# Kernel optimization log

Hardware: AMD Instinct MI355X
Metric: run time of the kernel (lower is better)

Reference implementation:

```python
import jax, jax.numpy as jnp
import numpy as np

NUM_HEADS = 16
HEAD_DIM = 64
MODEL_DIM = NUM_HEADS * HEAD_DIM  # 1024
N_TOKENS = 121
BATCH = 1024
DISTURB_HEADS = np.array([0, 3], dtype=int)


def setup_inputs() -> dict:
    key = jax.random.key(0)
    ks = jax.random.split(key, 8)
    scale = 1.0 / np.sqrt(MODEL_DIM)
    return {
        "query": jax.random.normal(ks[0], (BATCH, MODEL_DIM), dtype=jnp.float32),
        "key": jax.random.normal(ks[1], (BATCH, N_TOKENS, MODEL_DIM), dtype=jnp.float32),
        "value": jax.random.normal(ks[2], (BATCH, N_TOKENS, MODEL_DIM), dtype=jnp.float32),
        "Wq": jax.random.normal(ks[3], (MODEL_DIM, MODEL_DIM), dtype=jnp.float32) * scale,
        "bq": jnp.zeros((MODEL_DIM,), dtype=jnp.float32),
        "Wk": jax.random.normal(ks[4], (MODEL_DIM, MODEL_DIM), dtype=jnp.float32) * scale,
        "bk": jnp.zeros((MODEL_DIM,), dtype=jnp.float32),
        "Wv": jax.random.normal(ks[5], (MODEL_DIM, MODEL_DIM), dtype=jnp.float32) * scale,
        "bv": jnp.zeros((MODEL_DIM,), dtype=jnp.float32),
    }


def reference(query, key, value, Wq, bq, Wk, bk, Wv, bv):
    B, N, _ = key.shape
    H, d = NUM_HEADS, HEAD_DIM
    # Linear projections (plain GEMMs)
    q_proj = query @ Wq + bq            # [B, H*d]
    k_proj = key @ Wk + bk              # [B, N, H*d]
    v_proj = value @ Wv + bv            # [B, N, H*d]

    q = q_proj.reshape(B, H, d)         # [B, H, d]
    k = k_proj.reshape(B, N, H, d)      # [B, N, H, d]
    v = v_proj.reshape(B, N, H, d)

    # single-query scores per head: [B, H, N]
    scores = jnp.einsum('bhd,bnhd->bhn', q, k)
    # head-wise disturb override: masked heads get all-ones scores
    mask = jnp.zeros((H,), dtype=bool).at[DISTURB_HEADS].set(True)[None, :, None]
    scores = jnp.where(mask, jnp.ones_like(scores), scores)
    # note: original scales by sqrt(d * H), not sqrt(d)
    scores = scores / jnp.sqrt(jnp.asarray(d * H, dtype=scores.dtype))
    weights = jax.nn.softmax(scores, axis=-1)   # [B, H, N]
    output = jnp.einsum('bhn,bnhd->bhd', weights, v).reshape(B, H * d)
    return (output, weights)
```

## Files before the change

kernel.cpp:

```cpp
#include <hip/hip_runtime.h>
#include <hip/hip_bf16.h>

#define NHEADS 16
#define HDIM   64
#define MDIM   1024
#define NTOK   121
#define NBATCH 1024

typedef __attribute__((ext_vector_type(4))) float f32x4;
typedef __attribute__((ext_vector_type(4))) short s16x4;
typedef __attribute__((ext_vector_type(8))) short s16x8;

#define WAIT_VM(n)  asm volatile("s_waitcnt vmcnt(" #n ")" ::: "memory")
#define WAIT_LGKM0() asm volatile("s_waitcnt lgkmcnt(0)" ::: "memory")

__device__ __forceinline__ short f2bf(float f) {
  __hip_bfloat16 h = __float2bfloat16(f);
  return __builtin_bit_cast(short, h);
}

#define GLDS(gptr, lptr)                                                        \
  __builtin_amdgcn_global_load_lds(                                             \
      (const __attribute__((address_space(1))) void*)(gptr),                    \
      (__attribute__((address_space(3))) void*)(lptr), 16, 0, 0)

__global__ __launch_bounds__(256) void kTransW(const float* __restrict__ Wq,
                                               const float* __restrict__ Wk,
                                               const float* __restrict__ Wv,
                                               short* __restrict__ Wt) {
  int bid = blockIdx.x;
  int m = bid >> 8, tile = bid & 255;
  int tr = tile >> 4, tc = tile & 15;
  const float* W = (m == 0) ? Wq : (m == 1) ? Wk : Wv;
  short* T = Wt + (size_t)m * (MDIM * MDIM);
  __shared__ float tl[64][68];
  int t = threadIdx.x;
  int c4 = t & 15, r0 = t >> 4;
#pragma unroll
  for (int i = 0; i < 4; ++i) {
    int kr = r0 + i * 16;
    f32x4 v = *(const f32x4*)(W + (size_t)(tr * 64 + kr) * MDIM + tc * 64 + c4 * 4);
    *(f32x4*)&tl[kr][c4 * 4] = v;
  }
  __syncthreads();
#pragma unroll
  for (int i = 0; i < 4; ++i) {
    int n = r0 + i * 16;
    s16x4 o;
    o.x = f2bf(tl[c4 * 4 + 0][n]);
    o.y = f2bf(tl[c4 * 4 + 1][n]);
    o.z = f2bf(tl[c4 * 4 + 2][n]);
    o.w = f2bf(tl[c4 * 4 + 3][n]);
    *(s16x4*)(T + (size_t)(tc * 64 + n) * MDIM + tr * 64 + c4 * 4) = o;
  }
}

__device__ __forceinline__ void gemm_core(const float* __restrict__ A, int mrows,
                                          const short* __restrict__ Wt, int c0,
                                          short* Alds, short* Bl0, short* Bl1,
                                          f32x4 acc[4][4], int t) {
  int wid = t >> 6, lane = t & 63;
  int wr = wid >> 1, wc = wid & 1;
  int li = lane & 15, lg = lane >> 4;
  int kq = t & 15, r0s = t >> 4;
#pragma unroll
  for (int fm = 0; fm < 4; ++fm)
#pragma unroll
    for (int fn = 0; fn < 4; ++fn) acc[fm][fn] = (f32x4)0.0f;

  int rhi[4];
#pragma unroll
  for (int i = 0; i < 4; ++i) {
    int row = r0s + 64 + (i << 4);
    rhi[i] = row < mrows ? row : mrows - 1;
  }
#pragma unroll
  for (int i = 0; i < 4; ++i) {
    int cl = wid * 32 + i * 8 + (lane >> 3);
    int jg = (lane & 7) ^ (cl & 7);
    GLDS(Wt + (size_t)(c0 + cl) * MDIM + jg * 8, Bl0 + (wid * 32 + i * 8) * 64);
  }
  f32x4 rLo[4];
#pragma unroll
  for (int i = 0; i < 4; ++i)
    rLo[i] = *(const f32x4*)(A + (size_t)(r0s + (i << 4)) * MDIM + kq * 4);

  for (int kt = 0; kt < 16; ++kt) {
    int k0 = kt * 64;
    short* Bcur = (kt & 1) ? Bl1 : Bl0;
    short* Bnxt = (kt & 1) ? Bl0 : Bl1;
    int kn = (kt < 15) ? k0 + 64 : 0;

    f32x4 rHi[4];
#pragma unroll
    for (int i = 0; i < 4; ++i)
      rHi[i] = *(const f32x4*)(A + (size_t)rhi[i] * MDIM + k0 + kq * 4);

    WAIT_VM(4);
    __builtin_amdgcn_s_barrier();
#pragma unroll
    for (int i = 0; i < 4; ++i) {
      int row = r0s + (i << 4);
      s16x4 b4;
      b4.x = f2bf(rLo[i].x); b4.y = f2bf(rLo[i].y);
      b4.z = f2bf(rLo[i].z); b4.w = f2bf(rLo[i].w);
      int byte = (row * 128 + kq * 8) ^ ((row & 7) << 4);
      *(s16x4*)((char*)Alds + byte) = b4;
    }
#pragma unroll
    for (int i = 0; i < 4; ++i) {
      int cl = wid * 32 + i * 8 + (lane >> 3);
      int jg = (lane & 7) ^ (cl & 7);
      GLDS(Wt + (size_t)(c0 + cl) * MDIM + kn + jg * 8, Bnxt + (wid * 32 + i * 8) * 64);
    }
    WAIT_VM(4);
#pragma unroll
    for (int i = 0; i < 4; ++i) {
      int row = r0s + 64 + (i << 4);
      s16x4 b4;
      b4.x = f2bf(rHi[i].x); b4.y = f2bf(rHi[i].y);
      b4.z = f2bf(rHi[i].z); b4.w = f2bf(rHi[i].w);
      int byte = (row * 128 + kq * 8) ^ ((row & 7) << 4);
      *(s16x4*)((char*)Alds + byte) = b4;
    }
#pragma unroll
    for (int i = 0; i < 4; ++i)
      rLo[i] = *(const f32x4*)(A + (size_t)(r0s + (i << 4)) * MDIM + kn + kq * 4);

    WAIT_LGKM0();
    __builtin_amdgcn_s_barrier();
#pragma unroll
    for (int ks = 0; ks < 2; ++ks) {
      s16x8 af[4];
      int kb = ks * 64 + lg * 16;
#pragma unroll
      for (int fm = 0; fm < 4; ++fm) {
        int row = wr * 64 + fm * 16 + li;
        int byte = (row * 128 + kb) ^ ((row & 7) << 4);
        af[fm] = *(s16x8*)((char*)Alds + byte);
      }
#pragma unroll
      for (int fn = 0; fn < 4; ++fn) {
        int col = wc * 64 + fn * 16 + li;
        int byte = (col * 128 + kb) ^ ((col & 7) << 4);
        s16x8 bfv = *(s16x8*)((char*)Bcur + byte);
#pragma unroll
        for (int fm = 0; fm < 4; ++fm)
          acc[fm][fn] = __builtin_amdgcn_mfma_f32_16x16x32_bf16(af[fm], bfv,
                                                                acc[fm][fn], 0, 0, 0);
      }
    }
  }
}

__global__ __launch_bounds__(256, 3) void kQProj(const float* __restrict__ query,
                                                 const short* __restrict__ WtQ,
                                                 const float* __restrict__ bq,
                                                 float* __restrict__ qp) {
  __shared__ alignas(16) short Alds[128 * 64];
  __shared__ alignas(16) short Bl0[128 * 64];
  __shared__ alignas(16) short Bl1[128 * 64];
  int bid = blockIdx.x;
  int rt = bid >> 3, ct = bid & 7;
  f32x4 acc[4][4];
  int t = threadIdx.x;
  gemm_core(query + (size_t)rt * 128 * MDIM, 128, WtQ, ct * 128, Alds, Bl0, Bl1, acc, t);
  int wid = t >> 6, lane = t & 63;
  int wr = wid >> 1, wc = wid & 1, li = lane & 15, lg = lane >> 4;
#pragma unroll
  for (int fn = 0; fn < 4; ++fn) {
    int col = ct * 128 + wc * 64 + fn * 16 + li;
    float bqv = bq[col];
#pragma unroll
    for (int fm = 0; fm < 4; ++fm)
#pragma unroll
      for (int rr = 0; rr < 4; ++rr) {
        int row = rt * 128 + wr * 64 + fm * 16 + lg * 4 + rr;
        qp[(size_t)row * MDIM + col] = acc[fm][fn][rr] + bqv;
      }
  }
}

__global__ __launch_bounds__(256, 3) void kG(const float* __restrict__ qp,
                                             const short* __restrict__ WtK,
                                             short* __restrict__ g) {
  __shared__ alignas(16) short Alds[128 * 64];
  __shared__ alignas(16) short Blds[128 * 64];
  int bid = blockIdx.x;
  int h = bid >> 6, bt = (bid >> 3) & 7, it = bid & 7;
  int t = threadIdx.x;
  int wid = t >> 6, lane = t & 63;
  int wr = wid >> 1, wc = wid & 1, li = lane & 15, lg = lane >> 4;
  int kq = t & 15, r0s = t >> 4;
#pragma unroll
  for (int i = 0; i < 8; ++i) {
    int r = r0s + 16 * i;
    f32x4 v = *(const f32x4*)(qp + (size_t)(bt * 128 + r) * MDIM + h * 64 + kq * 4);
    s16x4 b4;
    b4.x = f2bf(v.x); b4.y = f2bf(v.y); b4.z = f2bf(v.z); b4.w = f2bf(v.w);
    int byte = (r * 128 + kq * 8) ^ ((r & 7) << 4);
    *(s16x4*)((char*)Alds + byte) = b4;
  }
  {
    int jr = t >> 2, qc = t & 3;
#pragma unroll
    for (int q = 0; q < 4; ++q) {
      s16x8 v = *(const s16x8*)(WtK + (size_t)(h * 64 + jr) * MDIM + it * 128 +
                                qc * 32 + q * 8);
#pragma unroll
      for (int e = 0; e < 8; ++e) {
        int i = qc * 32 + q * 8 + e;
        int byte = (i * 128 + jr * 2) ^ ((i & 7) << 4);
        *(short*)((char*)Blds + byte) = v[e];
      }
    }
  }
  __syncthreads();
  f32x4 acc[4][4];
#pragma unroll
  for (int fm = 0; fm < 4; ++fm)
#pragma unroll
    for (int fn = 0; fn < 4; ++fn) acc[fm][fn] = (f32x4)0.0f;
#pragma unroll
  for (int ks = 0; ks < 2; ++ks) {
    int kb = ks * 64 + lg * 16;
    s16x8 af[4];
#pragma unroll
    for (int fm = 0; fm < 4; ++fm) {
      int row = wr * 64 + fm * 16 + li;
      int byte = (row * 128 + kb) ^ ((row & 7) << 4);
      af[fm] = *(s16x8*)((char*)Alds + byte);
    }
#pragma unroll
    for (int fn = 0; fn < 4; ++fn) {
      int col = wc * 64 + fn * 16 + li;
      int byte = (col * 128 + kb) ^ ((col & 7) << 4);
      s16x8 bfv = *(s16x8*)((char*)Blds + byte);
#pragma unroll
      for (int fm = 0; fm < 4; ++fm)
        acc[fm][fn] = __builtin_amdgcn_mfma_f32_16x16x32_bf16(af[fm], bfv,
                                                              acc[fm][fn], 0, 0, 0);
    }
  }
#pragma unroll
  for (int fm = 0; fm < 4; ++fm)
#pragma unroll
    for (int rr = 0; rr < 4; ++rr) {
      int b = bt * 128 + wr * 64 + fm * 16 + lg * 4 + rr;
      short* gp = g + ((size_t)b * 16 + h) * 1024 + it * 128;
#pragma unroll
      for (int fn = 0; fn < 4; ++fn)
        gp[wc * 64 + fn * 16 + li] = f2bf(acc[fm][fn][rr]);
    }
}

__global__ __launch_bounds__(512, 4) void kWV(const float* __restrict__ key,
                                              const float* __restrict__ value,
                                              const short* __restrict__ g,
                                              float* __restrict__ weights,
                                              short* __restrict__ vbar) {
  __shared__ alignas(16) short Kl0[128 * 64];
  __shared__ alignas(16) short Kl1[128 * 64];
  __shared__ alignas(16) short Glds[16 * 1024];
  __shared__ float s_lds[16][132];
  int b = blockIdx.x;
  int t = threadIdx.x;
  int wid = t >> 6, lane = t & 63, li = lane & 15, lg = lane >> 4;
  int kq = t & 15, r0s = t >> 4;
  int rcl[4];
#pragma unroll
  for (int i = 0; i < 4; ++i) {
    int r = r0s + 32 * i;
    rcl[i] = r < NTOK ? r : NTOK - 1;
  }
  const float* A = key + (size_t)b * NTOK * MDIM;
  const short* gb = g + (size_t)b * 16384;
#pragma unroll
  for (int q = 0; q < 4; ++q) {
    int c = q * 512 + t;
    s16x8 v = *(const s16x8*)(gb + c * 8);
    int byte = ((c >> 7) * 2048 + (c & 127) * 16) ^ (((c >> 7) & 7) << 4);
    *(s16x8*)((char*)Glds + byte) = v;
  }
  f32x4 rA0[4], rA1[4], rA2[4], rA3[4];
#pragma unroll
  for (int i = 0; i < 4; ++i)
    rA0[i] = *(const f32x4*)(A + (size_t)rcl[i] * MDIM + 0 + kq * 4);
#pragma unroll
  for (int i = 0; i < 4; ++i)
    rA1[i] = *(const f32x4*)(A + (size_t)rcl[i] * MDIM + 64 + kq * 4);
#pragma unroll
  for (int i = 0; i < 4; ++i)
    rA2[i] = *(const f32x4*)(A + (size_t)rcl[i] * MDIM + 128 + kq * 4);
#pragma unroll
  for (int i = 0; i < 4; ++i)
    rA3[i] = *(const f32x4*)(A + (size_t)rcl[i] * MDIM + 192 + kq * 4);
  WAIT_LGKM0();
  __builtin_amdgcn_s_barrier();
  f32x4 acc = (f32x4)0.0f;

#define SCORE_STEP(S, RA, KL)                                                   \
  do {                                                                          \
    WAIT_VM(12);                                                                \
    _Pragma("unroll")                                                           \
    for (int i = 0; i < 4; ++i) {                                               \
      int row = r0s + 32 * i;                                                   \
      s16x4 b4;                                                                 \
      b4.x = f2bf(RA[i].x); b4.y = f2bf(RA[i].y);                               \
      b4.z = f2bf(RA[i].z); b4.w = f2bf(RA[i].w);                               \
      int byte = (row * 128 + kq * 8) ^ ((row & 7) << 4);                       \
      *(s16x4*)((char*)KL + byte) = b4;                                         \
    }                                                                           \
    {                                                                           \
      int kn = ((S) + 4 < 16) ? ((S) + 4) * 64 : 0;  \
      _Pragma("unroll")                                                         \
      for (int i = 0; i < 4; ++i)                                               \
        RA[i] = *(const f32x4*)(A + (size_t)rcl[i] * MDIM + kn + kq * 4);       \
    }                                                                           \
    WAIT_LGKM0();                                                               \
    __builtin_amdgcn_s_barrier();                                               \
    _Pragma("unroll")                                                           \
    for (int ks = 0; ks < 2; ++ks) {                                            \
      int kb = ks * 64 + lg * 16;                                               \
      int row = wid * 16 + li;                                                  \
      s16x8 af = *(s16x8*)((char*)KL + ((row * 128 + kb) ^ ((row & 7) << 4)));  \
      int kel = (S) * 64 + ks * 32 + lg * 8;                                    \
      s16x8 bf = *(s16x8*)((char*)Glds +                                        \
                           ((li * 2048 + kel * 2) ^ ((li & 7) << 4)));          \
      acc = __builtin_amdgcn_mfma_f32_16x16x32_bf16(af, bf, acc, 0, 0, 0);      \
    }                                                                           \
  } while (0)

  for (int sb = 0; sb < 16; sb += 4) {
    SCORE_STEP(sb + 0, rA0, Kl0);
    SCORE_STEP(sb + 1, rA1, Kl1);
    SCORE_STEP(sb + 2, rA2, Kl0);
    SCORE_STEP(sb + 3, rA3, Kl1);
  }
#undef SCORE_STEP

#pragma unroll
  for (int rr = 0; rr < 4; ++rr) s_lds[li][wid * 16 + lg * 4 + rr] = acc[rr];
  __syncthreads();
  float (*w_lds)[128] = (float(*)[128])Glds;
#pragma unroll
  for (int hh = 0; hh < 2; ++hh) {
    int h = wid * 2 + hh;
    int n0 = lane, n1 = lane + 64;
    bool v0 = (n0 < NTOK), v1 = (n1 < NTOK);
    float w0, w1;
    if (h == 0 || h == 3) {
      w0 = 1.f / NTOK; w1 = 1.f / NTOK;
    } else {
      const float kinv = 1.f / 32.f;
      float s0 = v0 ? s_lds[h][n0] * kinv : -1e30f;
      float s1 = v1 ? s_lds[h][n1] * kinv : -1e30f;
      float m = fmaxf(s0, s1);
#pragma unroll
      for (int msk = 1; msk < 64; msk <<= 1) m = fmaxf(m, __shfl_xor(m, msk));
      float e0 = v0 ? __expf(s0 - m) : 0.f;
      float e1 = v1 ? __expf(s1 - m) : 0.f;
      float s = e0 + e1;
#pragma unroll
      for (int msk = 1; msk < 64; msk <<= 1) s += __shfl_xor(s, msk);
      float inv = 1.f / s;
      w0 = e0 * inv; w1 = e1 * inv;
    }
    float* wp = weights + ((size_t)b * NHEADS + h) * NTOK;
    if (v0) { wp[n0] = w0; w_lds[h][n0] = w0; }
    if (v1) { wp[n1] = w1; w_lds[h][n1] = w1; }
  }
  __syncthreads();

  int grp = t >> 7, ic = t & 127;
  const float* V = value + (size_t)b * NTOK * MDIM;
  f32x4 a0[4], a1[4];
#pragma unroll
  for (int hh = 0; hh < 4; ++hh) { a0[hh] = (f32x4)0.0f; a1[hh] = (f32x4)0.0f; }
#pragma unroll 4
  for (int n = 0; n < NTOK; ++n) {
    f32x4 v0 = *(const f32x4*)(V + (size_t)n * MDIM + ic * 8);
    f32x4 v1 = *(const f32x4*)(V + (size_t)n * MDIM + ic * 8 + 4);
#pragma unroll
    for (int hh = 0; hh < 4; ++hh) {
      float wn = w_lds[grp * 4 + hh][n];
      a0[hh] += wn * v0;
      a1[hh] += wn * v1;
    }
  }
#pragma unroll
  for (int hh = 0; hh < 4; ++hh) {
    s16x8 o;
    o[0] = f2bf(a0[hh].x); o[1] = f2bf(a0[hh].y);
    o[2] = f2bf(a0[hh].z); o[3] = f2bf(a0[hh].w);
    o[4] = f2bf(a1[hh].x); o[5] = f2bf(a1[hh].y);
    o[6] = f2bf(a1[hh].z); o[7] = f2bf(a1[hh].w);
    *(s16x8*)(vbar + ((size_t)b * 16 + grp * 4 + hh) * 1024 + ic * 8) = o;
  }
}

__global__ __launch_bounds__(256, 3) void kO(const short* __restrict__ vbar,
                                             const short* __restrict__ WtV,
                                             const float* __restrict__ bv,
                                             float* __restrict__ outp) {
  __shared__ alignas(16) short Alds[128 * 64];
  __shared__ alignas(16) short Blds[64 * 64];
  int bid = blockIdx.x;
  int bt = bid >> 4, h = bid & 15;
  int t = threadIdx.x;
  int wid = t >> 6, lane = t & 63;
  int wr = wid >> 1, wc = wid & 1, li = lane & 15, lg = lane >> 4;
  f32x4 acc[4][2];
#pragma unroll
  for (int fm = 0; fm < 4; ++fm)
#pragma unroll
    for (int fn = 0; fn < 2; ++fn) acc[fm][fn] = (f32x4)0.0f;

  for (int kt = 0; kt < 16; ++kt) {
    int k0 = kt * 64;
    __syncthreads();
#pragma unroll
    for (int i = 0; i < 4; ++i) {
      int lrow = wid * 32 + i * 8 + (lane >> 3);
      int jg = (lane & 7) ^ (lrow & 7);
      GLDS(vbar + ((size_t)(bt * 128 + lrow) * 16 + h) * 1024 + k0 + jg * 8,
           Alds + (wid * 32 + i * 8) * 64);
    }
#pragma unroll
    for (int j = 0; j < 2; ++j) {
      int cl = wid * 16 + j * 8 + (lane >> 3);
      int jg = (lane & 7) ^ (cl & 7);
      GLDS(WtV + (size_t)(h * 64 + cl) * MDIM + k0 + jg * 8,
           Blds + (wid * 16 + j * 8) * 64);
    }
    __syncthreads();
#pragma unroll
    for (int ks = 0; ks < 2; ++ks) {
      int kb = ks * 64 + lg * 16;
      s16x8 af[4];
#pragma unroll
      for (int fm = 0; fm < 4; ++fm) {
        int row = wr * 64 + fm * 16 + li;
        int byte = (row * 128 + kb) ^ ((row & 7) << 4);
        af[fm] = *(s16x8*)((char*)Alds + byte);
      }
#pragma unroll
      for (int fn = 0; fn < 2; ++fn) {
        int col = wc * 32 + fn * 16 + li;
        int byte = (col * 128 + kb) ^ ((col & 7) << 4);
        s16x8 bfv = *(s16x8*)((char*)Blds + byte);
#pragma unroll
        for (int fm = 0; fm < 4; ++fm)
          acc[fm][fn] = __builtin_amdgcn_mfma_f32_16x16x32_bf16(af[fm], bfv,
                                                                acc[fm][fn], 0, 0, 0);
      }
    }
  }
#pragma unroll
  for (int fn = 0; fn < 2; ++fn) {
    int cg = h * 64 + wc * 32 + fn * 16 + li;
    float bvv = bv[cg];
#pragma unroll
    for (int fm = 0; fm < 4; ++fm)
#pragma unroll
      for (int rr = 0; rr < 4; ++rr) {
        int row = bt * 128 + wr * 64 + fm * 16 + lg * 4 + rr;
        outp[(size_t)row * MDIM + cg] = acc[fm][fn][rr] + bvv;
      }
  }
}

extern "C" void kernel_launch(void* const* d_in, const int* in_sizes, int n_in,
                              void* d_out, int out_size, void* d_ws, size_t ws_size,
                              hipStream_t stream) {
  const float* query = (const float*)d_in[0];
  const float* key   = (const float*)d_in[1];
  const float* value = (const float*)d_in[2];
  const float* Wq    = (const float*)d_in[3];
  const float* bq    = (const float*)d_in[4];
  const float* Wk    = (const float*)d_in[5];
  const float* bk    = (const float*)d_in[6];
  const float* Wv    = (const float*)d_in[7];
  const float* bv    = (const float*)d_in[8];
  (void)bk;

  float* out     = (float*)d_out;
  float* weights = out + (size_t)NBATCH * MDIM;

  char* ws = (char*)d_ws;
  short* Wt   = (short*)ws;
  float* qp   = (float*)(ws + 6u  * 1024 * 1024);
  short* g    = (short*)(ws + 10u * 1024 * 1024);
  short* vbar = (short*)(ws + 48u * 1024 * 1024);

  kTransW<<<dim3(768),  dim3(256), 0, stream>>>(Wq, Wk, Wv, Wt);
  kQProj <<<dim3(64),   dim3(256), 0, stream>>>(query, Wt, bq, qp);
  kG     <<<dim3(1024), dim3(256), 0, stream>>>(qp, Wt + (size_t)MDIM * MDIM, g);
  kWV    <<<dim3(1024), dim3(512), 0, stream>>>(key, value, g, weights, vbar);
  kO     <<<dim3(128),  dim3(256), 0, stream>>>(vbar, Wt + 2 * (size_t)MDIM * MDIM,
                                                bv, out);
}
```

Before: 317.1 us.

## Load key and g fragments directly from global in kWV score phase, drop LDS staging

Replaces the LDS-staged, double-buffered key tile and the g buffer held in LDS with direct per-lane global loads of key rows and g fragments, which are converted to bf16 in registers and fed to the MFMA. This removes about 64KB of shared memory and the per-step barriers, so launch bounds are raised to allow more resident blocks per CU. The cost is uncoalesced, strided global access patterns, redundant g reads across waves, and no explicit prefetch pipelining. The padding of w_lds is now zeroed explicitly.

```diff
diff --git a/kernel.cpp b/kernel.cpp
--- a/kernel.cpp
+++ b/kernel.cpp
@@ -254,95 +254,38 @@
     }
 }
 
-__global__ __launch_bounds__(512, 4) void kWV(const float* __restrict__ key,
+__global__ __launch_bounds__(512, 6) void kWV(const float* __restrict__ key,
                                               const float* __restrict__ value,
                                               const short* __restrict__ g,
                                               float* __restrict__ weights,
                                               short* __restrict__ vbar) {
-  __shared__ alignas(16) short Kl0[128 * 64];
-  __shared__ alignas(16) short Kl1[128 * 64];
-  __shared__ alignas(16) short Glds[16 * 1024];
   __shared__ float s_lds[16][132];
+  __shared__ float w_lds[16][128];
   int b = blockIdx.x;
   int t = threadIdx.x;
   int wid = t >> 6, lane = t & 63, li = lane & 15, lg = lane >> 4;
-  int kq = t & 15, r0s = t >> 4;
-  int rcl[4];
-#pragma unroll
-  for (int i = 0; i < 4; ++i) {
-    int r = r0s + 32 * i;
-    rcl[i] = r < NTOK ? r : NTOK - 1;
-  }
-  const float* A = key + (size_t)b * NTOK * MDIM;
-  const short* gb = g + (size_t)b * 16384;
-#pragma unroll
-  for (int q = 0; q < 4; ++q) {
-    int c = q * 512 + t;
-    s16x8 v = *(const s16x8*)(gb + c * 8);
-    int byte = ((c >> 7) * 2048 + (c & 127) * 16) ^ (((c >> 7) & 7) << 4);
-    *(s16x8*)((char*)Glds + byte) = v;
-  }
-  f32x4 rA0[4], rA1[4], rA2[4], rA3[4];
-#pragma unroll
-  for (int i = 0; i < 4; ++i)
-    rA0[i] = *(const f32x4*)(A + (size_t)rcl[i] * MDIM + 0 + kq * 4);
-#pragma unroll
-  for (int i = 0; i < 4; ++i)
-    rA1[i] = *(const f32x4*)(A + (size_t)rcl[i] * MDIM + 64 + kq * 4);
-#pragma unroll
-  for (int i = 0; i < 4; ++i)
-    rA2[i] = *(const f32x4*)(A + (size_t)rcl[i] * MDIM + 128 + kq * 4);
-#pragma unroll
-  for (int i = 0; i < 4; ++i)
-    rA3[i] = *(const f32x4*)(A + (size_t)rcl[i] * MDIM + 192 + kq * 4);
-  WAIT_LGKM0();
-  __builtin_amdgcn_s_barrier();
+  int tr = wid * 16 + li;
+  if (tr >= NTOK) tr = NTOK - 1;
+  const float* Arow = key + ((size_t)b * NTOK + tr) * MDIM;
+  const short* grow = g + (size_t)b * 16384 + li * 1024;
+
   f32x4 acc = (f32x4)0.0f;
-
-#define SCORE_STEP(S, RA, KL)                                                   \
-  do {                                                                          \
-    WAIT_VM(12);                                                                \
-    _Pragma("unroll")                                                           \
-    for (int i = 0; i < 4; ++i) {                                               \
-      int row = r0s + 32 * i;                                                   \
-      s16x4 b4;                                                                 \
-      b4.x = f2bf(RA[i].x); b4.y = f2bf(RA[i].y);                               \
-      b4.z = f2bf(RA[i].z); b4.w = f2bf(RA[i].w);                               \
-      int byte = (row * 128 + kq * 8) ^ ((row & 7) << 4);                       \
-      *(s16x4*)((char*)KL + byte) = b4;                                         \
-    }                                                                           \
-    {                                                                           \
-      int kn = ((S) + 4 < 16) ? ((S) + 4) * 64 : 0;  \
-      _Pragma("unroll")                                                         \
-      for (int i = 0; i < 4; ++i)                                               \
-        RA[i] = *(const f32x4*)(A + (size_t)rcl[i] * MDIM + kn + kq * 4);       \
-    }                                                                           \
-    WAIT_LGKM0();                                                               \
-    __builtin_amdgcn_s_barrier();                                               \
-    _Pragma("unroll")                                                           \
-    for (int ks = 0; ks < 2; ++ks) {                                            \
-      int kb = ks * 64 + lg * 16;                                               \
-      int row = wid * 16 + li;                                                  \
-      s16x8 af = *(s16x8*)((char*)KL + ((row * 128 + kb) ^ ((row & 7) << 4)));  \
-      int kel = (S) * 64 + ks * 32 + lg * 8;                                    \
-      s16x8 bf = *(s16x8*)((char*)Glds +                                        \
-                           ((li * 2048 + kel * 2) ^ ((li & 7) << 4)));          \
-      acc = __builtin_amdgcn_mfma_f32_16x16x32_bf16(af, bf, acc, 0, 0, 0);      \
-    }                                                                           \
-  } while (0)
-
-  for (int sb = 0; sb < 16; sb += 4) {
-    SCORE_STEP(sb + 0, rA0, Kl0);
-    SCORE_STEP(sb + 1, rA1, Kl1);
-    SCORE_STEP(sb + 2, rA2, Kl0);
-    SCORE_STEP(sb + 3, rA3, Kl1);
-  }
-#undef SCORE_STEP
-
+  for (int S = 0; S < 16; ++S) {
+#pragma unroll
+    for (int ks = 0; ks < 2; ++ks) {
+      int ko = S * 64 + ks * 32 + lg * 8;
+      f32x4 k0 = *(const f32x4*)(Arow + ko);
+      f32x4 k1 = *(const f32x4*)(Arow + ko + 4);
+      s16x8 bf = *(const s16x8*)(grow + ko);
+      s16x8 af;
+      af[0] = f2bf(k0.x); af[1] = f2bf(k0.y); af[2] = f2bf(k0.z); af[3] = f2bf(k0.w);
+      af[4] = f2bf(k1.x); af[5] = f2bf(k1.y); af[6] = f2bf(k1.z); af[7] = f2bf(k1.w);
+      acc = __builtin_amdgcn_mfma_f32_16x16x32_bf16(af, bf, acc, 0, 0, 0);
+    }
+  }
 #pragma unroll
   for (int rr = 0; rr < 4; ++rr) s_lds[li][wid * 16 + lg * 4 + rr] = acc[rr];
   __syncthreads();
-  float (*w_lds)[128] = (float(*)[128])Glds;
 #pragma unroll
   for (int hh = 0; hh < 2; ++hh) {
     int h = wid * 2 + hh;
@@ -369,6 +312,7 @@
     float* wp = weights + ((size_t)b * NHEADS + h) * NTOK;
     if (v0) { wp[n0] = w0; w_lds[h][n0] = w0; }
     if (v1) { wp[n1] = w1; w_lds[h][n1] = w1; }
+    if (lane < 7) w_lds[h][NTOK + lane] = 0.f;
   }
   __syncthreads();
 
```

After: 554.5 us. +74.9%, slower.
